# Kernel tuning notes

Measured on AMD Instinct MI355X. Metric: run time of the kernel, lower is better.

The kernel has to match this reference:

```python
import jax, jax.numpy as jnp
import numpy as np


def _mlp2(x, W1, b1, W2, b2):
    # ReluMLP with two Dense layers: relu between layers, linear output
    return jax.nn.relu(x @ W1 + b1) @ W2 + b2


def setup_inputs() -> dict:
    key = jax.random.key(0)
    N, NP, DIN, D = 100000, 25000, 16, 64
    E, EDS, EP, EUS = 1_600_000, 800_000, 400_000, 200_000
    L = 8  # number of message-passing layers actually used
    ks = iter(jax.random.split(key, 40))
    nrm = lambda shape: jax.random.normal(next(ks), shape, jnp.float32) * 0.05
    ri = lambda n, hi: jax.random.randint(next(ks), (n,), 0, hi)
    return dict(
        x=jax.random.normal(next(ks), (N, DIN), jnp.float32),
        We1=nrm((DIN, D)), be1=jnp.zeros((D,), jnp.float32),
        We2=nrm((D, D)), be2=jnp.zeros((D,), jnp.float32),
        Wm1=nrm((L, D, D)), bm1=jnp.zeros((L, D), jnp.float32),
        Wm2=nrm((L, D, D)), bm2=jnp.zeros((L, D), jnp.float32),
        Wn1=nrm((L, 2 * D, D)), bn1=jnp.zeros((L, D), jnp.float32),
        Wn2=nrm((L, D, D)), bn2=jnp.zeros((L, D), jnp.float32),
        Wd1=nrm((D, D)), bd1=jnp.zeros((D,), jnp.float32),
        Wd2=nrm((D, 2)), bd2=jnp.zeros((2,), jnp.float32),
        s_fine=ri(E, N), r_fine=ri(E, N),
        s_ds=ri(EDS, N), r_ds=ri(EDS, N),
        s_p=ri(EP, NP), r_p=ri(EP, NP),
        s_us=ri(EUS, NP), r_us=ri(EUS, NP),
        uppool=ri(N, NP), downpool=ri(NP, NP),
    )


def reference(x, We1, be1, We2, be2, Wm1, bm1, Wm2, bm2, Wn1, bn1, Wn2, bn2,
              Wd1, bd1, Wd2, bd2, s_fine, r_fine, s_ds, r_ds, s_p, r_p,
              s_us, r_us, uppool, downpool):
    def mp(l, h, s, r, n):
        # LinearMessagePassingLayer: message MLP on sender feats,
        # sum-scatter to receivers (mean_aggr=False), node MLP on [h, aggr]
        msg = _mlp2(h[s], Wm1[l], bm1[l], Wm2[l], bm2[l])          # [E, D]
        aggr = jax.ops.segment_sum(msg, r, num_segments=n)          # [n, D]
        return _mlp2(jnp.concatenate([h, aggr], -1),
                     Wn1[l], bn1[l], Wn2[l], bn2[l])                # [n, D]

    N = x.shape[0]
    NP = downpool.shape[0]
    # encode
    h = _mlp2(x, We1, be1, We2, be2)                                 # [N, D]
    h = mp(0, h, s_fine, r_fine, N)
    h = mp(1, h, s_fine, r_fine, N)
    skip = h
    # Downsample: gather by uppool idx, MP on downsampling graph, select pooled
    g = mp(2, h[uppool], s_ds, r_ds, N)                              # [N, D]
    hp = g[downpool]                                                 # [NP, D]
    # bottleneck
    hp = mp(3, hp, s_p, r_p, NP)
    hp = mp(4, hp, s_p, r_p, NP)
    # Upsample: gather by downpool idx, MP on upsampling graph, select by uppool
    g = mp(5, hp[downpool], s_us, r_us, NP)                          # [NP, D]
    h = g[uppool]                                                    # [N, D]
    # decode with skip connections
    h = mp(6, h, s_fine, r_fine, N) + skip
    h = mp(7, h, s_fine, r_fine, N) + skip
    return _mlp2(h, Wd1, bd1, Wd2, bd2)                              # [N, 2]
```

## Files before the change

### kernel.cpp

```cpp
#include <hip/hip_runtime.h>

#define WG 256

#define MLP_FMA16(ACC, A, W) do { \
    ACC[0][0]=fmaf(A.x,W.x,ACC[0][0]); ACC[0][1]=fmaf(A.x,W.y,ACC[0][1]); \
    ACC[0][2]=fmaf(A.x,W.z,ACC[0][2]); ACC[0][3]=fmaf(A.x,W.w,ACC[0][3]); \
    ACC[1][0]=fmaf(A.y,W.x,ACC[1][0]); ACC[1][1]=fmaf(A.y,W.y,ACC[1][1]); \
    ACC[1][2]=fmaf(A.y,W.z,ACC[1][2]); ACC[1][3]=fmaf(A.y,W.w,ACC[1][3]); \
    ACC[2][0]=fmaf(A.z,W.x,ACC[2][0]); ACC[2][1]=fmaf(A.z,W.y,ACC[2][1]); \
    ACC[2][2]=fmaf(A.z,W.z,ACC[2][2]); ACC[2][3]=fmaf(A.z,W.w,ACC[2][3]); \
    ACC[3][0]=fmaf(A.w,W.x,ACC[3][0]); ACC[3][1]=fmaf(A.w,W.y,ACC[3][1]); \
    ACC[3][2]=fmaf(A.w,W.z,ACC[3][2]); ACC[3][3]=fmaf(A.w,W.w,ACC[3][3]); \
} while (0)

template<int DINA, bool HAS_B, bool HAS_SKIP, bool GATHER_A,
         int MSG_DOUT, bool PARTIAL_MSG, bool WRITE_OUT1>
__global__ __launch_bounds__(WG)
void mlp2_fused(const float* __restrict__ inA, const int* __restrict__ gidxA,
                const float* __restrict__ inB,
                const float* __restrict__ W1, const float* __restrict__ b1,
                const float* __restrict__ W2, const float* __restrict__ b2,
                const float* __restrict__ skip, float* __restrict__ out1,
                const float* __restrict__ M1, const float* __restrict__ mb1,
                const float* __restrict__ M2, const float* __restrict__ mb2,
                float* __restrict__ outM, int msgN, int n)
{
    constexpr int DIN = DINA + (HAS_B ? 64 : 0);
    constexpr int XROWS = (DIN > 64) ? DIN : 64;
    constexpr int XP = 68;
    __shared__ __align__(16) float sXT[XROWS][XP];
    __shared__ __align__(16) float sW[64 * 64];
    __shared__ float sb[128];
    __shared__ float sW2d[128];
    __shared__ float sb2d[2];

    const int tid = threadIdx.x;
    const int tx = tid & 15, ty = tid >> 4;
    const int c0 = tx * 4, r0 = ty * 4;
    const int row0 = blockIdx.x * 64;

    constexpr int K1 = (DIN > 64) ? 64 : DIN;
    for (int i = tid * 4; i < K1 * 64; i += WG * 4)
        *(float4*)&sW[i] = *(const float4*)&W1[i];
    if (tid < 64) sb[tid] = b1[tid];
    else if (tid < 128) sb[tid] = b2[tid - 64];

    {
        const int lrow = tid & 63;
        const int kq0 = (tid >> 6) * 4;
        const int rg = min(row0 + lrow, n - 1);
        const int ra = GATHER_A ? gidxA[rg] : rg;
        const float* pA = inA + (size_t)ra * DINA;
        #pragma unroll
        for (int kq = kq0; kq < DINA; kq += 16) {
            const float4 v = *(const float4*)(pA + kq);
            sXT[kq + 0][lrow] = v.x; sXT[kq + 1][lrow] = v.y;
            sXT[kq + 2][lrow] = v.z; sXT[kq + 3][lrow] = v.w;
        }
        if (HAS_B) {
            const float* pB = inB + (size_t)rg * 64;
            #pragma unroll
            for (int kq = kq0; kq < 64; kq += 16) {
                const float4 v = *(const float4*)(pB + kq);
                sXT[DINA + kq + 0][lrow] = v.x; sXT[DINA + kq + 1][lrow] = v.y;
                sXT[DINA + kq + 2][lrow] = v.z; sXT[DINA + kq + 3][lrow] = v.w;
            }
        }
    }
    __syncthreads();

    float acc[4][4] = {};
    #pragma unroll 8
    for (int k = 0; k < K1; ++k) {
        const float4 a = *(const float4*)&sXT[k][r0];
        const float4 w = *(const float4*)&sW[k * 64 + c0];
        MLP_FMA16(acc, a, w);
    }
    if constexpr (DIN > 64) {
        __syncthreads();
        for (int i = tid * 4; i < 64 * 64; i += WG * 4)
            *(float4*)&sW[i] = *(const float4*)&W1[64 * 64 + i];
        __syncthreads();
        #pragma unroll 8
        for (int kk = 0; kk < 64; ++kk) {
            const float4 a = *(const float4*)&sXT[64 + kk][r0];
            const float4 w = *(const float4*)&sW[kk * 64 + c0];
            MLP_FMA16(acc, a, w);
        }
    }
    __syncthreads();

    for (int i = tid * 4; i < 64 * 64; i += WG * 4)
        *(float4*)&sW[i] = *(const float4*)&W2[i];
    #pragma unroll
    for (int j = 0; j < 4; ++j) {
        const float bj = sb[c0 + j];
        float4 hv = make_float4(fmaxf(acc[0][j] + bj, 0.0f),
                                fmaxf(acc[1][j] + bj, 0.0f),
                                fmaxf(acc[2][j] + bj, 0.0f),
                                fmaxf(acc[3][j] + bj, 0.0f));
        *(float4*)&sXT[c0 + j][r0] = hv;
    }
    __syncthreads();

    float acc2[4][4] = {};
    #pragma unroll 8
    for (int k = 0; k < 64; ++k) {
        const float4 a = *(const float4*)&sXT[k][r0];
        const float4 w = *(const float4*)&sW[k * 64 + c0];
        MLP_FMA16(acc2, a, w);
    }

    float ofull[4][4];
    #pragma unroll
    for (int i = 0; i < 4; ++i) {
        const int row = row0 + r0 + i;
        float4 s = make_float4(0.f, 0.f, 0.f, 0.f);
        if (HAS_SKIP && row < n) s = *(const float4*)&skip[(size_t)row * 64 + c0];
        ofull[i][0] = acc2[i][0] + sb[64 + c0 + 0] + s.x;
        ofull[i][1] = acc2[i][1] + sb[64 + c0 + 1] + s.y;
        ofull[i][2] = acc2[i][2] + sb[64 + c0 + 2] + s.z;
        ofull[i][3] = acc2[i][3] + sb[64 + c0 + 3] + s.w;
        if (WRITE_OUT1 && row < n)
            *(float4*)&out1[(size_t)row * 64 + c0] =
                make_float4(ofull[i][0], ofull[i][1], ofull[i][2], ofull[i][3]);
    }

    if constexpr (MSG_DOUT > 0) {
        if (!PARTIAL_MSG || row0 < msgN) {
            __syncthreads();
            for (int i = tid * 4; i < 64 * 64; i += WG * 4)
                *(float4*)&sW[i] = *(const float4*)&M1[i];
            if (tid < 64) sb[tid] = mb1[tid];
            if constexpr (MSG_DOUT == 64) {
                if (tid >= 64 && tid < 128) sb[tid] = mb2[tid - 64];
            } else {
                if (tid >= 64 && tid < 192) sW2d[tid - 64] = M2[tid - 64];
                if (tid >= 192 && tid < 194) sb2d[tid - 192] = mb2[tid - 192];
            }
            #pragma unroll
            for (int j = 0; j < 4; ++j)
                *(float4*)&sXT[c0 + j][r0] =
                    make_float4(ofull[0][j], ofull[1][j], ofull[2][j], ofull[3][j]);
            __syncthreads();

            float acc3[4][4] = {};
            #pragma unroll 8
            for (int k = 0; k < 64; ++k) {
                const float4 a = *(const float4*)&sXT[k][r0];
                const float4 w = *(const float4*)&sW[k * 64 + c0];
                MLP_FMA16(acc3, a, w);
            }
            __syncthreads();
            if constexpr (MSG_DOUT == 64) {
                for (int i = tid * 4; i < 64 * 64; i += WG * 4)
                    *(float4*)&sW[i] = *(const float4*)&M2[i];
            }
            #pragma unroll
            for (int j = 0; j < 4; ++j) {
                const float bj = sb[c0 + j];
                float4 hv = make_float4(fmaxf(acc3[0][j] + bj, 0.0f),
                                        fmaxf(acc3[1][j] + bj, 0.0f),
                                        fmaxf(acc3[2][j] + bj, 0.0f),
                                        fmaxf(acc3[3][j] + bj, 0.0f));
                *(float4*)&sXT[c0 + j][r0] = hv;
            }
            __syncthreads();

            if constexpr (MSG_DOUT == 64) {
                float accM[4][4] = {};
                #pragma unroll 8
                for (int k = 0; k < 64; ++k) {
                    const float4 a = *(const float4*)&sXT[k][r0];
                    const float4 w = *(const float4*)&sW[k * 64 + c0];
                    MLP_FMA16(accM, a, w);
                }
                #pragma unroll
                for (int i = 0; i < 4; ++i) {
                    const int row = row0 + r0 + i;
                    if (row < msgN)
                        *(float4*)&outM[(size_t)row * 64 + c0] =
                            make_float4(accM[i][0] + sb[64 + c0 + 0],
                                        accM[i][1] + sb[64 + c0 + 1],
                                        accM[i][2] + sb[64 + c0 + 2],
                                        accM[i][3] + sb[64 + c0 + 3]);
                }
            } else {
                if (tid < 128) {
                    const int lr = tid >> 1, col = tid & 1;
                    float o0 = sb2d[col], o1 = 0.0f;
                    #pragma unroll 8
                    for (int k = 0; k < 64; k += 2) {
                        o0 = fmaf(sXT[k][lr],     sW2d[k * 2 + col],       o0);
                        o1 = fmaf(sXT[k + 1][lr], sW2d[(k + 1) * 2 + col], o1);
                    }
                    const int row = row0 + lr;
                    if (row < msgN) outM[(size_t)row * 2 + col] = o0 + o1;
                }
            }
        }
    }
}

template<int DINA, bool HAS_B, bool HAS_SKIP, bool GATHER_A>
__global__ __launch_bounds__(WG)
void mlp2_rt(const float* __restrict__ inA, const int* __restrict__ gidxA,
             const float* __restrict__ inB,
             const float* __restrict__ W1, const float* __restrict__ b1,
             const float* __restrict__ W2, const float* __restrict__ b2,
             const float* __restrict__ skip,
             float* __restrict__ out, int n)
{
    constexpr int DIN = DINA + (HAS_B ? 64 : 0);
    constexpr int XROWS = (DIN > 64) ? DIN : 64;
    constexpr int XP = 68;
    __shared__ __align__(16) float sXT[XROWS][XP];
    __shared__ __align__(16) float sW[64 * 64];
    __shared__ float sb[128];

    const int tid = threadIdx.x;
    const int tx = tid & 15, ty = tid >> 4;
    const int c0 = tx * 4, r0 = ty * 4;
    const int row0 = blockIdx.x * 64;

    constexpr int K1 = (DIN > 64) ? 64 : DIN;
    for (int i = tid * 4; i < K1 * 64; i += WG * 4)
        *(float4*)&sW[i] = *(const float4*)&W1[i];
    if (tid < 64) sb[tid] = b1[tid];
    else if (tid < 128) sb[tid] = b2[tid - 64];

    {
        const int lrow = tid & 63;
        const int kq0 = (tid >> 6) * 4;
        const int rg = min(row0 + lrow, n - 1);
        const int ra = GATHER_A ? gidxA[rg] : rg;
        const float* pA = inA + (size_t)ra * DINA;
        #pragma unroll
        for (int kq = kq0; kq < DINA; kq += 16) {
            const float4 v = *(const float4*)(pA + kq);
            sXT[kq + 0][lrow] = v.x; sXT[kq + 1][lrow] = v.y;
            sXT[kq + 2][lrow] = v.z; sXT[kq + 3][lrow] = v.w;
        }
        if (HAS_B) {
            const float* pB = inB + (size_t)rg * 64;
            #pragma unroll
            for (int kq = kq0; kq < 64; kq += 16) {
                const float4 v = *(const float4*)(pB + kq);
                sXT[DINA + kq + 0][lrow] = v.x; sXT[DINA + kq + 1][lrow] = v.y;
                sXT[DINA + kq + 2][lrow] = v.z; sXT[DINA + kq + 3][lrow] = v.w;
            }
        }
    }
    __syncthreads();

    float acc[4][4] = {};
    #pragma unroll 8
    for (int k = 0; k < K1; ++k) {
        const float4 a = *(const float4*)&sXT[k][r0];
        const float4 w = *(const float4*)&sW[k * 64 + c0];
        MLP_FMA16(acc, a, w);
    }
    if constexpr (DIN > 64) {
        __syncthreads();
        for (int i = tid * 4; i < 64 * 64; i += WG * 4)
            *(float4*)&sW[i] = *(const float4*)&W1[64 * 64 + i];
        __syncthreads();
        #pragma unroll 8
        for (int kk = 0; kk < 64; ++kk) {
            const float4 a = *(const float4*)&sXT[64 + kk][r0];
            const float4 w = *(const float4*)&sW[kk * 64 + c0];
            MLP_FMA16(acc, a, w);
        }
    }
    __syncthreads();

    for (int i = tid * 4; i < 64 * 64; i += WG * 4)
        *(float4*)&sW[i] = *(const float4*)&W2[i];
    #pragma unroll
    for (int j = 0; j < 4; ++j) {
        const float bj = sb[c0 + j];
        float4 hv = make_float4(fmaxf(acc[0][j] + bj, 0.0f),
                                fmaxf(acc[1][j] + bj, 0.0f),
                                fmaxf(acc[2][j] + bj, 0.0f),
                                fmaxf(acc[3][j] + bj, 0.0f));
        *(float4*)&sXT[c0 + j][r0] = hv;
    }
    __syncthreads();

    float acc2[4][4] = {};
    #pragma unroll 8
    for (int k = 0; k < 64; ++k) {
        const float4 a = *(const float4*)&sXT[k][r0];
        const float4 w = *(const float4*)&sW[k * 64 + c0];
        MLP_FMA16(acc2, a, w);
    }
    #pragma unroll
    for (int i = 0; i < 4; ++i) {
        const int row = row0 + r0 + i;
        if (row < n) {
            float4 o = make_float4(acc2[i][0] + sb[64 + c0 + 0],
                                   acc2[i][1] + sb[64 + c0 + 1],
                                   acc2[i][2] + sb[64 + c0 + 2],
                                   acc2[i][3] + sb[64 + c0 + 3]);
            if (HAS_SKIP) {
                const float4 s = *(const float4*)&skip[(size_t)row * 64 + c0];
                o.x += s.x; o.y += s.y; o.z += s.z; o.w += s.w;
            }
            *(float4*)&out[(size_t)row * 64 + c0] = o;
        }
    }
}

__global__ __launch_bounds__(WG)
void slot_fill_xcd_k(const int* __restrict__ s, const int* __restrict__ r,
                     int* __restrict__ cursor, int* __restrict__ slots,
                     int cap, int E, int n)
{
    const int xcd = blockIdx.x & 7;
    const int w   = blockIdx.x >> 3;
    const int W   = gridDim.x >> 3;
    const int lo  = (int)(((long)n * xcd) >> 3);
    const int hi  = (int)(((long)n * (xcd + 1)) >> 3);
    const int chunk = (E + W - 1) / W;
    const int e0 = w * chunk;
    const int e1 = min(E, e0 + chunk);
    for (int e = e0 + (int)threadIdx.x; e < e1; e += WG) {
        const int v = __builtin_nontemporal_load(&r[e]);
        if (v >= lo && v < hi) {
            const int sv = __builtin_nontemporal_load(&s[e]);
            const int p = atomicAdd(&cursor[v], 1);
            if (p < cap) slots[(size_t)v * cap + p] = sv;
        }
    }
}

template<bool REMAP>
__global__ __launch_bounds__(WG)
void gather_slots_k(const int* __restrict__ deg, const int* __restrict__ slots,
                    int cap, const int* __restrict__ remap,
                    const float* __restrict__ tab, float* __restrict__ aggr, int n)
{
    const int node = blockIdx.x * (WG / 64) + (threadIdx.x >> 6);
    const int c = threadIdx.x & 63;
    if (node >= n) return;
    const int d = min(deg[node], cap);
    const int* sl = slots + (size_t)node * cap;

    int myidx = 0;
    if (c < d) {
        myidx = __builtin_nontemporal_load(&sl[c]);
        if (REMAP) myidx = remap[myidx];
    }

    float a[8] = {};
    int j = 0;
    for (; j + 7 < d; j += 8) {
        #pragma unroll
        for (int u = 0; u < 8; ++u) {
            const int t = __shfl(myidx, j + u);
            a[u] += tab[(size_t)t * 64 + c];
        }
    }
    #pragma unroll 4
    for (; j < d; ++j) {
        const int t = __shfl(myidx, j);
        a[j & 7] += tab[(size_t)t * 64 + c];
    }
    aggr[(size_t)node * 64 + c] =
        ((a[0] + a[1]) + (a[2] + a[3])) + ((a[4] + a[5]) + (a[6] + a[7]));
}

extern "C" void kernel_launch(void* const* d_in, const int* in_sizes, int n_in,
                              void* d_out, int out_size, void* d_ws, size_t ws_size,
                              hipStream_t stream)
{
    const float* x    = (const float*)d_in[0];
    const float* We1  = (const float*)d_in[1];
    const float* be1  = (const float*)d_in[2];
    const float* We2  = (const float*)d_in[3];
    const float* be2  = (const float*)d_in[4];
    const float* Wm1  = (const float*)d_in[5];
    const float* bm1  = (const float*)d_in[6];
    const float* Wm2  = (const float*)d_in[7];
    const float* bm2  = (const float*)d_in[8];
    const float* Wn1  = (const float*)d_in[9];
    const float* bn1  = (const float*)d_in[10];
    const float* Wn2  = (const float*)d_in[11];
    const float* bn2  = (const float*)d_in[12];
    const float* Wd1  = (const float*)d_in[13];
    const float* bd1  = (const float*)d_in[14];
    const float* Wd2  = (const float*)d_in[15];
    const float* bd2  = (const float*)d_in[16];
    const int* s_fine = (const int*)d_in[17];
    const int* r_fine = (const int*)d_in[18];
    const int* s_ds   = (const int*)d_in[19];
    const int* r_ds   = (const int*)d_in[20];
    const int* s_p    = (const int*)d_in[21];
    const int* r_p    = (const int*)d_in[22];
    const int* s_us   = (const int*)d_in[23];
    const int* r_us   = (const int*)d_in[24];
    const int* uppool   = (const int*)d_in[25];
    const int* downpool = (const int*)d_in[26];

    const int N   = in_sizes[0] / 16;
    const int E   = in_sizes[17];
    const int EDS = in_sizes[19];
    const int EP  = in_sizes[21];
    const int EUS = in_sizes[23];
    const int NP  = in_sizes[26];

    const int CAP_FINE = 48, CAP_DS = 32, CAP_PP = 48, CAP_US = 32;

    float* B0  = (float*)d_ws;
    float* B1  = B0 + (size_t)N * 64;
    float* B2  = B1 + (size_t)N * 64;
    float* B3  = B2 + (size_t)N * 64;
    float* HPa = B3 + (size_t)N * 64;
    float* HPb = HPa + (size_t)NP * 64;
    int* ip = (int*)(HPb + (size_t)NP * 64);
    auto alloc_i = [&](size_t n) { int* p = ip; ip += n; return p; };
    int* cur_fine = alloc_i(N);
    int* cur_ds   = alloc_i(N);
    int* cur_pp   = alloc_i(NP);
    int* cur_us   = alloc_i(NP);
    int* sl_fine  = alloc_i((size_t)N * CAP_FINE);
    int* sl_ds    = alloc_i((size_t)N * CAP_DS);
    int* sl_pp    = alloc_i((size_t)NP * CAP_PP);
    int* sl_us    = alloc_i((size_t)NP * CAP_US);

    const int gN  = (N + 63) / 64;
    const int gNP = (NP + 63) / 64;
    const int gaN  = (N + 3) / 4;
    const int gaNP = (NP + 3) / 4;

    hipMemsetAsync(cur_fine, 0, (size_t)(2 * N + 2 * NP) * sizeof(int), stream);
    slot_fill_xcd_k<<<2048, WG, 0, stream>>>(s_fine, r_fine, cur_fine, sl_fine, CAP_FINE, E,   N);
    slot_fill_xcd_k<<<1024, WG, 0, stream>>>(s_ds,   r_ds,   cur_ds,   sl_ds,   CAP_DS,   EDS, N);
    slot_fill_xcd_k<<<512,  WG, 0, stream>>>(s_p,    r_p,    cur_pp,   sl_pp,   CAP_PP,   EP,  NP);
    slot_fill_xcd_k<<<512,  WG, 0, stream>>>(s_us,   r_us,   cur_us,   sl_us,   CAP_US,   EUS, NP);

    mlp2_fused<16,false,false,false,64,false,true><<<gN,WG,0,stream>>>(
        x,nullptr,nullptr, We1,be1,We2,be2, nullptr,B0,
        Wm1+0*4096,bm1+0*64,Wm2+0*4096,bm2+0*64, B1, N, N);
    gather_slots_k<false><<<gaN,WG,0,stream>>>(cur_fine,sl_fine,CAP_FINE,nullptr,B1,B2,N);

    mlp2_fused<64,true,false,false,64,false,true><<<gN,WG,0,stream>>>(
        B0,nullptr,B2, Wn1+0*8192,bn1+0*64,Wn2+0*4096,bn2+0*64, nullptr,B3,
        Wm1+1*4096,bm1+1*64,Wm2+1*4096,bm2+1*64, B0, N, N);
    gather_slots_k<false><<<gaN,WG,0,stream>>>(cur_fine,sl_fine,CAP_FINE,nullptr,B0,B2,N);

    mlp2_fused<64,true,false,false,64,true,true><<<gN,WG,0,stream>>>(
        B3,nullptr,B2, Wn1+1*8192,bn1+1*64,Wn2+1*4096,bn2+1*64, nullptr,B1,
        Wm1+2*4096,bm1+2*64,Wm2+2*4096,bm2+2*64, B0, NP, N);
    gather_slots_k<true><<<gaN,WG,0,stream>>>(cur_ds,sl_ds,CAP_DS,uppool,B0,B2,N);

    mlp2_rt<64,true,false,true><<<gN,WG,0,stream>>>(
        B1,uppool,B2, Wn1+2*8192,bn1+2*64,Wn2+2*4096,bn2+2*64, nullptr,B3,N);

    mlp2_rt<64,false,false,true><<<gNP,WG,0,stream>>>(
        B3,downpool,nullptr, Wm1+3*4096,bm1+3*64,Wm2+3*4096,bm2+3*64, nullptr,HPa,NP);
    gather_slots_k<false><<<gaNP,WG,0,stream>>>(cur_pp,sl_pp,CAP_PP,nullptr,HPa,B2,NP);

    mlp2_fused<64,true,false,true,64,false,true><<<gNP,WG,0,stream>>>(
        B3,downpool,B2, Wn1+3*8192,bn1+3*64,Wn2+3*4096,bn2+3*64, nullptr,HPb,
        Wm1+4*4096,bm1+4*64,Wm2+4*4096,bm2+4*64, HPa, NP, NP);
    gather_slots_k<false><<<gaNP,WG,0,stream>>>(cur_pp,sl_pp,CAP_PP,nullptr,HPa,B2,NP);

    mlp2_fused<64,true,false,false,64,false,true><<<gNP,WG,0,stream>>>(
        HPb,nullptr,B2, Wn1+4*8192,bn1+4*64,Wn2+4*4096,bn2+4*64, nullptr,HPa,
        Wm1+5*4096,bm1+5*64,Wm2+5*4096,bm2+5*64, HPb, NP, NP);
    gather_slots_k<true><<<gaNP,WG,0,stream>>>(cur_us,sl_us,CAP_US,downpool,HPb,B2,NP);

    mlp2_fused<64,true,false,true,64,false,true><<<gNP,WG,0,stream>>>(
        HPa,downpool,B2, Wn1+5*8192,bn1+5*64,Wn2+5*4096,bn2+5*64, nullptr,HPb,
        Wm1+6*4096,bm1+6*64,Wm2+6*4096,bm2+6*64, B3, NP, NP);
    gather_slots_k<true><<<gaN,WG,0,stream>>>(cur_fine,sl_fine,CAP_FINE,uppool,B3,B2,N);

    mlp2_fused<64,true,true,true,64,false,true><<<gN,WG,0,stream>>>(
        HPb,uppool,B2, Wn1+6*8192,bn1+6*64,Wn2+6*4096,bn2+6*64, B1,B0,
        Wm1+7*4096,bm1+7*64,Wm2+7*4096,bm2+7*64, B3, N, N);
    gather_slots_k<false><<<gaN,WG,0,stream>>>(cur_fine,sl_fine,CAP_FINE,nullptr,B3,B2,N);

    mlp2_fused<64,true,true,false,2,false,false><<<gN,WG,0,stream>>>(
        B0,nullptr,B2, Wn1+7*8192,bn1+7*64,Wn2+7*4096,bn2+7*64, B1,nullptr,
        Wd1,bd1,Wd2,bd2, (float*)d_out, N, N);
}
```

Measured before the change: 1.091 ms.

## Enlarge MLP row tile to 128 rows with 8x4 register blocking

The fused MLP kernels now process 128 rows per workgroup instead of 64, with each thread computing an 8x4 output micro-tile so every weight value loaded from shared memory is reused across twice as many rows. The transposed activation buffer is restructured to 64x132, and the concatenated [h, aggr] input is handled in two phases: the first half is consumed before the second half is loaded into the same buffer. This halves weight-staging traffic per row and the number of workgroups. In exchange it raises register pressure, which may cut occupancy, and the grid for NP-sized launches becomes small.

```diff
diff --git a/kernel.cpp b/kernel.cpp
--- a/kernel.cpp
+++ b/kernel.cpp
@@ -2,15 +2,15 @@
 
 #define WG 256
 
-#define MLP_FMA16(ACC, A, W) do { \
-    ACC[0][0]=fmaf(A.x,W.x,ACC[0][0]); ACC[0][1]=fmaf(A.x,W.y,ACC[0][1]); \
-    ACC[0][2]=fmaf(A.x,W.z,ACC[0][2]); ACC[0][3]=fmaf(A.x,W.w,ACC[0][3]); \
-    ACC[1][0]=fmaf(A.y,W.x,ACC[1][0]); ACC[1][1]=fmaf(A.y,W.y,ACC[1][1]); \
-    ACC[1][2]=fmaf(A.y,W.z,ACC[1][2]); ACC[1][3]=fmaf(A.y,W.w,ACC[1][3]); \
-    ACC[2][0]=fmaf(A.z,W.x,ACC[2][0]); ACC[2][1]=fmaf(A.z,W.y,ACC[2][1]); \
-    ACC[2][2]=fmaf(A.z,W.z,ACC[2][2]); ACC[2][3]=fmaf(A.z,W.w,ACC[2][3]); \
-    ACC[3][0]=fmaf(A.w,W.x,ACC[3][0]); ACC[3][1]=fmaf(A.w,W.y,ACC[3][1]); \
-    ACC[3][2]=fmaf(A.w,W.z,ACC[3][2]); ACC[3][3]=fmaf(A.w,W.w,ACC[3][3]); \
+#define MLP_FMA_ROW(ACC_ROW, AV, W) \
+    ACC_ROW[0]=fmaf(AV,W.x,ACC_ROW[0]); ACC_ROW[1]=fmaf(AV,W.y,ACC_ROW[1]); \
+    ACC_ROW[2]=fmaf(AV,W.z,ACC_ROW[2]); ACC_ROW[3]=fmaf(AV,W.w,ACC_ROW[3]);
+
+#define MLP_FMA8(ACC, A0, A1, W) do { \
+    MLP_FMA_ROW(ACC[0], A0.x, W) MLP_FMA_ROW(ACC[1], A0.y, W) \
+    MLP_FMA_ROW(ACC[2], A0.z, W) MLP_FMA_ROW(ACC[3], A0.w, W) \
+    MLP_FMA_ROW(ACC[4], A1.x, W) MLP_FMA_ROW(ACC[5], A1.y, W) \
+    MLP_FMA_ROW(ACC[6], A1.z, W) MLP_FMA_ROW(ACC[7], A1.w, W) \
 } while (0)
 
 template<int DINA, bool HAS_B, bool HAS_SKIP, bool GATHER_A,
@@ -25,10 +25,8 @@
                 const float* __restrict__ M2, const float* __restrict__ mb2,
                 float* __restrict__ outM, int msgN, int n)
 {
-    constexpr int DIN = DINA + (HAS_B ? 64 : 0);
-    constexpr int XROWS = (DIN > 64) ? DIN : 64;
-    constexpr int XP = 68;
-    __shared__ __align__(16) float sXT[XROWS][XP];
+    constexpr int XP = 132;
+    __shared__ __align__(16) float sXT[64][XP];
     __shared__ __align__(16) float sW[64 * 64];
     __shared__ float sb[128];
     __shared__ float sW2d[128];
@@ -36,56 +34,61 @@
 
     const int tid = threadIdx.x;
     const int tx = tid & 15, ty = tid >> 4;
-    const int c0 = tx * 4, r0 = ty * 4;
-    const int row0 = blockIdx.x * 64;
-
-    constexpr int K1 = (DIN > 64) ? 64 : DIN;
-    for (int i = tid * 4; i < K1 * 64; i += WG * 4)
+    const int c0 = tx * 4, r0 = ty * 8;
+    const int row0 = blockIdx.x * 128;
+    const int lrow = tid & 127;
+    const int kq0 = (tid >> 7) * 4;
+
+    for (int i = tid * 4; i < DINA * 64; i += WG * 4)
         *(float4*)&sW[i] = *(const float4*)&W1[i];
     if (tid < 64) sb[tid] = b1[tid];
     else if (tid < 128) sb[tid] = b2[tid - 64];
 
     {
-        const int lrow = tid & 63;
-        const int kq0 = (tid >> 6) * 4;
         const int rg = min(row0 + lrow, n - 1);
         const int ra = GATHER_A ? gidxA[rg] : rg;
         const float* pA = inA + (size_t)ra * DINA;
         #pragma unroll
-        for (int kq = kq0; kq < DINA; kq += 16) {
+        for (int t = 0; t < DINA / 8; ++t) {
+            const int kq = kq0 + t * 8;
             const float4 v = *(const float4*)(pA + kq);
             sXT[kq + 0][lrow] = v.x; sXT[kq + 1][lrow] = v.y;
             sXT[kq + 2][lrow] = v.z; sXT[kq + 3][lrow] = v.w;
         }
-        if (HAS_B) {
+    }
+    __syncthreads();
+
+    float acc[8][4] = {};
+    #pragma unroll 4
+    for (int k = 0; k < DINA; ++k) {
+        const float4 a0 = *(const float4*)&sXT[k][r0];
+        const float4 a1 = *(const float4*)&sXT[k][r0 + 4];
+        const float4 w  = *(const float4*)&sW[k * 64 + c0];
+        MLP_FMA8(acc, a0, a1, w);
+    }
+
+    if constexpr (HAS_B) {
+        __syncthreads();
+        for (int i = tid * 4; i < 64 * 64; i += WG * 4)
+            *(float4*)&sW[i] = *(const float4*)&W1[DINA * 64 + i];
+        {
+            const int rg = min(row0 + lrow, n - 1);
             const float* pB = inB + (size_t)rg * 64;
             #pragma unroll
-            for (int kq = kq0; kq < 64; kq += 16) {
+            for (int t = 0; t < 8; ++t) {
+                const int kq = kq0 + t * 8;
                 const float4 v = *(const float4*)(pB + kq);
-                sXT[DINA + kq + 0][lrow] = v.x; sXT[DINA + kq + 1][lrow] = v.y;
-                sXT[DINA + kq + 2][lrow] = v.z; sXT[DINA + kq + 3][lrow] = v.w;
-            }
-        }
-    }
-    __syncthreads();
-
-    float acc[4][4] = {};
-    #pragma unroll 8
-    for (int k = 0; k < K1; ++k) {
-        const float4 a = *(const float4*)&sXT[k][r0];
-        const float4 w = *(const float4*)&sW[k * 64 + c0];
-        MLP_FMA16(acc, a, w);
-    }
-    if constexpr (DIN > 64) {
+                sXT[kq + 0][lrow] = v.x; sXT[kq + 1][lrow] = v.y;
+                sXT[kq + 2][lrow] = v.z; sXT[kq + 3][lrow] = v.w;
+            }
+        }
         __syncthreads();
-        for (int i = tid * 4; i < 64 * 64; i += WG * 4)
-            *(float4*)&sW[i] = *(const float4*)&W1[64 * 64 + i];
-        __syncthreads();
-        #pragma unroll 8
-        for (int kk = 0; kk < 64; ++kk) {
-            const float4 a = *(const float4*)&sXT[64 + kk][r0];
-            const float4 w = *(const float4*)&sW[kk * 64 + c0];
-            MLP_FMA16(acc, a, w);
+        #pragma unroll 4
+        for (int k = 0; k < 64; ++k) {
+            const float4 a0 = *(const float4*)&sXT[k][r0];
+            const float4 a1 = *(const float4*)&sXT[k][r0 + 4];
+            const float4 w  = *(const float4*)&sW[k * 64 + c0];
+            MLP_FMA8(acc, a0, a1, w);
         }
     }
     __syncthreads();
@@ -95,25 +98,27 @@
     #pragma unroll
     for (int j = 0; j < 4; ++j) {
         const float bj = sb[c0 + j];
-        float4 hv = make_float4(fmaxf(acc[0][j] + bj, 0.0f),
-                                fmaxf(acc[1][j] + bj, 0.0f),
-                                fmaxf(acc[2][j] + bj, 0.0f),
-                                fmaxf(acc[3][j] + bj, 0.0f));
-        *(float4*)&sXT[c0 + j][r0] = hv;
+        *(float4*)&sXT[c0 + j][r0] = make_float4(
+            fmaxf(acc[0][j] + bj, 0.f), fmaxf(acc[1][j] + bj, 0.f),
+            fmaxf(acc[2][j] + bj, 0.f), fmaxf(acc[3][j] + bj, 0.f));
+        *(float4*)&sXT[c0 + j][r0 + 4] = make_float4(
+            fmaxf(acc[4][j] + bj, 0.f), fmaxf(acc[5][j] + bj, 0.f),
+            fmaxf(acc[6][j] + bj, 0.f), fmaxf(acc[7][j] + bj, 0.f));
     }
     __syncthreads();
 
-    float acc2[4][4] = {};
-    #pragma unroll 8
+    float acc2[8][4] = {};
+    #pragma unroll 4
     for (int k = 0; k < 64; ++k) {
-        const float4 a = *(const float4*)&sXT[k][r0];
-        const float4 w = *(const float4*)&sW[k * 64 + c0];
-        MLP_FMA16(acc2, a, w);
-    }
-
-    float ofull[4][4];
+        const float4 a0 = *(const float4*)&sXT[k][r0];
+        const float4 a1 = *(const float4*)&sXT[k][r0 + 4];
+        const float4 w  = *(const float4*)&sW[k * 64 + c0];
+        MLP_FMA8(acc2, a0, a1, w);
+    }
+
+    float ofull[8][4];
     #pragma unroll
-    for (int i = 0; i < 4; ++i) {
+    for (int i = 0; i < 8; ++i) {
         const int row = row0 + r0 + i;
         float4 s = make_float4(0.f, 0.f, 0.f, 0.f);
         if (HAS_SKIP && row < n) s = *(const float4*)&skip[(size_t)row * 64 + c0];
@@ -139,17 +144,21 @@
                 if (tid >= 192 && tid < 194) sb2d[tid - 192] = mb2[tid - 192];
             }
             #pragma unroll
-            for (int j = 0; j < 4; ++j)
+            for (int j = 0; j < 4; ++j) {
                 *(float4*)&sXT[c0 + j][r0] =
                     make_float4(ofull[0][j], ofull[1][j], ofull[2][j], ofull[3][j]);
+                *(float4*)&sXT[c0 + j][r0 + 4] =
+                    make_float4(ofull[4][j], ofull[5][j], ofull[6][j], ofull[7][j]);
+            }
             __syncthreads();
 
-            float acc3[4][4] = {};
-            #pragma unroll 8
+            float acc3[8][4] = {};
+            #pragma unroll 4
             for (int k = 0; k < 64; ++k) {
-                const float4 a = *(const float4*)&sXT[k][r0];
-                const float4 w = *(const float4*)&sW[k * 64 + c0];
-                MLP_FMA16(acc3, a, w);
+                const float4 a0 = *(const float4*)&sXT[k][r0];
+                const float4 a1 = *(const float4*)&sXT[k][r0 + 4];
+                const float4 w  = *(const float4*)&sW[k * 64 + c0];
+                MLP_FMA8(acc3, a0, a1, w);
             }
             __syncthreads();
             if constexpr (MSG_DOUT == 64) {
@@ -159,24 +168,26 @@
             #pragma unroll
             for (int j = 0; j < 4; ++j) {
                 const float bj = sb[c0 + j];
-                float4 hv = make_float4(fmaxf(acc3[0][j] + bj, 0.0f),
-                                        fmaxf(acc3[1][j] + bj, 0.0f),
-                                        fmaxf(acc3[2][j] + bj, 0.0f),
-                                        fmaxf(acc3[3][j] + bj, 0.0f));
-                *(float4*)&sXT[c0 + j][r0] = hv;
+                *(float4*)&sXT[c0 + j][r0] = make_float4(
+                    fmaxf(acc3[0][j] + bj, 0.f), fmaxf(acc3[1][j] + bj, 0.f),
+                    fmaxf(acc3[2][j] + bj, 0.f), fmaxf(acc3[3][j] + bj, 0.f));
+                *(float4*)&sXT[c0 + j][r0 + 4] = make_float4(
+                    fmaxf(acc3[4][j] + bj, 0.f), fmaxf(acc3[5][j] + bj, 0.f),
+                    fmaxf(acc3[6][j] + bj, 0.f), fmaxf(acc3[7][j] + bj, 0.f));
             }
             __syncthreads();
 
             if constexpr (MSG_DOUT == 64) {
-                float accM[4][4] = {};
-                #pragma unroll 8
+                float accM[8][4] = {};
+                #pragma unroll 4
                 for (int k = 0; k < 64; ++k) {
-                    const float4 a = *(const float4*)&sXT[k][r0];
-                    const float4 w = *(const float4*)&sW[k * 64 + c0];
-                    MLP_FMA16(accM, a, w);
+                    const float4 a0 = *(const float4*)&sXT[k][r0];
+                    const float4 a1 = *(const float4*)&sXT[k][r0 + 4];
+                    const float4 w  = *(const float4*)&sW[k * 64 + c0];
+                    MLP_FMA8(accM, a0, a1, w);
                 }
                 #pragma unroll
-                for (int i = 0; i < 4; ++i) {
+                for (int i = 0; i < 8; ++i) {
                     const int row = row0 + r0 + i;
                     if (row < msgN)
                         *(float4*)&outM[(size_t)row * 64 + c0] =
@@ -186,17 +197,15 @@
                                         accM[i][3] + sb[64 + c0 + 3]);
                 }
             } else {
-                if (tid < 128) {
-                    const int lr = tid >> 1, col = tid & 1;
-                    float o0 = sb2d[col], o1 = 0.0f;
-                    #pragma unroll 8
-                    for (int k = 0; k < 64; k += 2) {
-                        o0 = fmaf(sXT[k][lr],     sW2d[k * 2 + col],       o0);
-                        o1 = fmaf(sXT[k + 1][lr], sW2d[(k + 1) * 2 + col], o1);
-                    }
-                    const int row = row0 + lr;
-                    if (row < msgN) outM[(size_t)row * 2 + col] = o0 + o1;
+                const int lr = tid >> 1, col = tid & 1;
+                float o0 = sb2d[col], o1 = 0.0f;
+                #pragma unroll 8
+                for (int k = 0; k < 64; k += 2) {
+                    o0 = fmaf(sXT[k][lr],     sW2d[k * 2 + col],       o0);
+                    o1 = fmaf(sXT[k + 1][lr], sW2d[(k + 1) * 2 + col], o1);
                 }
+                const int row = row0 + lr;
+                if (row < msgN) outM[(size_t)row * 2 + col] = o0 + o1;
             }
         }
     }
@@ -211,65 +220,67 @@
              const float* __restrict__ skip,
              float* __restrict__ out, int n)
 {
-    constexpr int DIN = DINA + (HAS_B ? 64 : 0);
-    constexpr int XROWS = (DIN > 64) ? DIN : 64;
-    constexpr int XP = 68;
-    __shared__ __align__(16) float sXT[XROWS][XP];
+    constexpr int XP = 132;
+    __shared__ __align__(16) float sXT[64][XP];
     __shared__ __align__(16) float sW[64 * 64];
     __shared__ float sb[128];
 
     const int tid = threadIdx.x;
     const int tx = tid & 15, ty = tid >> 4;
-    const int c0 = tx * 4, r0 = ty * 4;
-    const int row0 = blockIdx.x * 64;
-
-    constexpr int K1 = (DIN > 64) ? 64 : DIN;
-    for (int i = tid * 4; i < K1 * 64; i += WG * 4)
+    const int c0 = tx * 4, r0 = ty * 8;
+    const int row0 = blockIdx.x * 128;
+    const int lrow = tid & 127;
+    const int kq0 = (tid >> 7) * 4;
+
+    for (int i = tid * 4; i < DINA * 64; i += WG * 4)
         *(float4*)&sW[i] = *(const float4*)&W1[i];
     if (tid < 64) sb[tid] = b1[tid];
     else if (tid < 128) sb[tid] = b2[tid - 64];
 
     {
-        const int lrow = tid & 63;
-        const int kq0 = (tid >> 6) * 4;
         const int rg = min(row0 + lrow, n - 1);
         const int ra = GATHER_A ? gidxA[rg] : rg;
         const float* pA = inA + (size_t)ra * DINA;
         #pragma unroll
-        for (int kq = kq0; kq < DINA; kq += 16) {
+        for (int t = 0; t < DINA / 8; ++t) {
+            const int kq = kq0 + t * 8;
             const float4 v = *(const float4*)(pA + kq);
             sXT[kq + 0][lrow] = v.x; sXT[kq + 1][lrow] = v.y;
             sXT[kq + 2][lrow] = v.z; sXT[kq + 3][lrow] = v.w;
         }
-        if (HAS_B) {
+    }
+    __syncthreads();
+
+    float acc[8][4] = {};
+    #pragma unroll 4
+    for (int k = 0; k < DINA; ++k) {
+        const float4 a0 = *(const float4*)&sXT[k][r0];
+        const float4 a1 = *(const float4*)&sXT[k][r0 + 4];
+        const float4 w  = *(const float4*)&sW[k * 64 + c0];
+        MLP_FMA8(acc, a0, a1, w);
+    }
+    if constexpr (HAS_B) {
+        __syncthreads();
+        for (int i = tid * 4; i < 64 * 64; i += WG * 4)
+            *(float4*)&sW[i] = *(const float4*)&W1[DINA * 64 + i];
+        {
+            const int rg = min(row0 + lrow, n - 1);
             const float* pB = inB + (size_t)rg * 64;
             #pragma unroll
-            for (int kq = kq0; kq < 64; kq += 16) {
+            for (int t = 0; t < 8; ++t) {
+                const int kq = kq0 + t * 8;
                 const float4 v = *(const float4*)(pB + kq);
-                sXT[DINA + kq + 0][lrow] = v.x; sXT[DINA + kq + 1][lrow] = v.y;
-                sXT[DINA + kq + 2][lrow] = v.z; sXT[DINA + kq + 3][lrow] = v.w;
-            }
-        }
-    }
-    __syncthreads();
-
-    float acc[4][4] = {};
-    #pragma unroll 8
-    for (int k = 0; k < K1; ++k) {
-        const float4 a = *(const float4*)&sXT[k][r0];
-        const float4 w = *(const float4*)&sW[k * 64 + c0];
-        MLP_FMA16(acc, a, w);
-    }
-    if constexpr (DIN > 64) {
+                sXT[kq + 0][lrow] = v.x; sXT[kq + 1][lrow] = v.y;
+                sXT[kq + 2][lrow] = v.z; sXT[kq + 3][lrow] = v.w;
+            }
+        }
         __syncthreads();
-        for (int i = tid * 4; i < 64 * 64; i += WG * 4)
-            *(float4*)&sW[i] = *(const float4*)&W1[64 * 64 + i];
-        __syncthreads();
-        #pragma unroll 8
-        for (int kk = 0; kk < 64; ++kk) {
-            const float4 a = *(const float4*)&sXT[64 + kk][r0];
-            const float4 w = *(const float4*)&sW[kk * 64 + c0];
-            MLP_FMA16(acc, a, w);
+        #pragma unroll 4
+        for (int k = 0; k < 64; ++k) {
+            const float4 a0 = *(const float4*)&sXT[k][r0];
+            const float4 a1 = *(const float4*)&sXT[k][r0 + 4];
+            const float4 w  = *(const float4*)&sW[k * 64 + c0];
+            MLP_FMA8(acc, a0, a1, w);
         }
     }
     __syncthreads();
@@ -279,23 +290,25 @@
     #pragma unroll
     for (int j = 0; j < 4; ++j) {
         const float bj = sb[c0 + j];
-        float4 hv = make_float4(fmaxf(acc[0][j] + bj, 0.0f),
-                                fmaxf(acc[1][j] + bj, 0.0f),
-                                fmaxf(acc[2][j] + bj, 0.0f),
-                                fmaxf(acc[3][j] + bj, 0.0f));
-        *(float4*)&sXT[c0 + j][r0] = hv;
+        *(float4*)&sXT[c0 + j][r0] = make_float4(
+            fmaxf(acc[0][j] + bj, 0.f), fmaxf(acc[1][j] + bj, 0.f),
+            fmaxf(acc[2][j] + bj, 0.f), fmaxf(acc[3][j] + bj, 0.f));
+        *(float4*)&sXT[c0 + j][r0 + 4] = make_float4(
+            fmaxf(acc[4][j] + bj, 0.f), fmaxf(acc[5][j] + bj, 0.f),
+            fmaxf(acc[6][j] + bj, 0.f), fmaxf(acc[7][j] + bj, 0.f));
     }
     __syncthreads();
 
-    float acc2[4][4] = {};
-    #pragma unroll 8
+    float acc2[8][4] = {};
+    #pragma unroll 4
     for (int k = 0; k < 64; ++k) {
-        const float4 a = *(const float4*)&sXT[k][r0];
-        const float4 w = *(const float4*)&sW[k * 64 + c0];
-        MLP_FMA16(acc2, a, w);
+        const float4 a0 = *(const float4*)&sXT[k][r0];
+        const float4 a1 = *(const float4*)&sXT[k][r0 + 4];
+        const float4 w  = *(const float4*)&sW[k * 64 + c0];
+        MLP_FMA8(acc2, a0, a1, w);
     }
     #pragma unroll
-    for (int i = 0; i < 4; ++i) {
+    for (int i = 0; i < 8; ++i) {
         const int row = row0 + r0 + i;
         if (row < n) {
             float4 o = make_float4(acc2[i][0] + sb[64 + c0 + 0],
@@ -428,8 +441,8 @@
     int* sl_pp    = alloc_i((size_t)NP * CAP_PP);
     int* sl_us    = alloc_i((size_t)NP * CAP_US);
 
-    const int gN  = (N + 63) / 64;
-    const int gNP = (NP + 63) / 64;
+    const int gN  = (N + 127) / 128;
+    const int gNP = (NP + 127) / 128;
     const int gaN  = (N + 3) / 4;
     const int gaNP = (NP + 3) / 4;
 
```

Result: slower. 1.127 ms (+3.3%).
